# Performance work log

Measured on AMD Instinct MI355X. Metric: run time of the kernel, lower is better.

Reference implementation:

```python
import jax, jax.numpy as jnp
import numpy as np

EPS = 1e-12

def _normalize(x, axis=-1):
    # matches torch F.normalize(dim=-1) with default eps=1e-12
    n = jnp.linalg.norm(x, axis=axis, keepdims=True)
    return x / jnp.maximum(n, EPS)

def setup_inputs() -> dict:
    key = jax.random.key(0)
    k1, k2, k3 = jax.random.split(key, 3)
    B, D, C = 262144, 256, 128
    dirs = jax.random.normal(k1, (B, D), dtype=jnp.float32)
    v_class = _normalize(jax.random.normal(k2, (C, D), dtype=jnp.float32))
    labels = jax.random.randint(k3, (B,), 0, C, dtype=jnp.int32)
    return {"dirs": dirs, "v_class": v_class, "labels": labels, "step": 100}

def reference(dirs, v_class, labels, step):
    n_classes, _ = v_class.shape
    ema_alpha = 0.02
    proto_weight = 0.1

    dirs_n = _normalize(dirs)                      # (B, D)

    # ---- EMA update (no-grad in original; segment-mean per class) ----
    d = jax.lax.stop_gradient(dirs_n)
    sums = jax.ops.segment_sum(d, labels, num_segments=n_classes)      # (C, D)
    counts = jax.ops.segment_sum(jnp.ones((d.shape[0],), d.dtype), labels,
                                 num_segments=n_classes)               # (C,)
    batch_mean = sums / jnp.maximum(counts, 1.0)[:, None]
    batch_mean = _normalize(batch_mean)
    alpha = min(ema_alpha, step / (step + 50))
    updated = _normalize((1.0 - alpha) * v_class + alpha * batch_mean)
    new_v = jnp.where((counts > 0)[:, None], updated, v_class)         # (C, D)
    new_v = jax.lax.stop_gradient(new_v)  # buffer: no grad flows through it

    # ---- prototype alignment loss ----
    protos = new_v[labels]                          # (B, D) gather
    cos_sim = jnp.sum(dirs_n * protos, axis=-1)     # (B,)
    l_proto = jnp.mean(1.0 - cos_sim)
    return proto_weight * l_proto, new_v
```

## Files before the change

### kernel.cpp

```cpp
#include <hip/hip_runtime.h>


#define PF_D 256
#define PF_C 128
#define PF_SCALE 524288.0f
#define PF_INV_SCALE (1.0f / 524288.0f)

__device__ __forceinline__ float pf_wave_sum(float v) {
  #pragma unroll
  for (int m = 1; m < 64; m <<= 1) v += __shfl_xor(v, m, 64);
  return v;
}

__global__ void pf_zero(int* __restrict__ ws, int n) {
  int i = blockIdx.x * blockDim.x + threadIdx.x;
  if (i < n) ws[i] = 0;
}

__global__ __launch_bounds__(1024) void pf_accum(
    const float* __restrict__ dirs, const int* __restrict__ labels,
    int* __restrict__ gsum, int* __restrict__ gcnt, int B) {
  __shared__ int lacc[PF_C * PF_D];
  __shared__ int lnum[PF_C];
  const int tid = threadIdx.x;
  for (int i = tid; i < PF_C * PF_D; i += 1024) lacc[i] = 0;
  if (tid < PF_C) lnum[tid] = 0;
  __syncthreads();

  const int lane = tid & 63;
  const int wave = tid >> 6;
  const int rows_per_block = (B + (int)gridDim.x - 1) / (int)gridDim.x;
  const int row_lo = blockIdx.x * rows_per_block;
  const int row_hi = min(B, row_lo + rows_per_block);

  for (int r = row_lo + wave; r < row_hi; r += 16) {
    float4 v = ((const float4*)(dirs + (size_t)r * PF_D))[lane];
    float sq = v.x * v.x + v.y * v.y + v.z * v.z + v.w * v.w;
    sq = pf_wave_sum(sq);
    float k = PF_SCALE / fmaxf(sqrtf(sq), 1e-12f);
    int cls = labels[r];
    int* p = lacc + cls * PF_D;
    atomicAdd(p + lane,       __float2int_rn(v.x * k));
    atomicAdd(p + 64  + lane, __float2int_rn(v.y * k));
    atomicAdd(p + 128 + lane, __float2int_rn(v.z * k));
    atomicAdd(p + 192 + lane, __float2int_rn(v.w * k));
    if (lane == 0) atomicAdd(&lnum[cls], 1);
  }
  __syncthreads();

  for (int i = tid; i < PF_C * PF_D; i += 1024) {
    int s = lacc[i];
    if (s != 0) atomicAdd(&gsum[i], s);
  }
  if (tid < PF_C) {
    int s = lnum[tid];
    if (s != 0) atomicAdd(&gcnt[tid], s);
  }
}

__global__ __launch_bounds__(256) void pf_final(
    const int* __restrict__ gsum, const int* __restrict__ gcnt,
    const float* __restrict__ v_class, const int* __restrict__ step_ptr,
    float* __restrict__ out, int B) {
  const int lane = threadIdx.x & 63;
  const int wave = threadIdx.x >> 6;
  const float stepf = (float)step_ptr[0];
  const float alpha = fminf(0.02f, stepf / (stepf + 50.f));
  float acc = 0.f;

  for (int c = wave; c < PF_C; c += 4) {
    int   cnt   = gcnt[c];
    float denom = fmaxf((float)cnt, 1.f);
    float s[4], vc[4], bm[4];
    float nb = 0.f;
    #pragma unroll
    for (int j = 0; j < 4; j++) {
      int e = lane + 64 * j;
      s[j]  = (float)gsum[c * PF_D + ((e & 3) << 6) + (e >> 2)] * PF_INV_SCALE;
      vc[j] = v_class[c * PF_D + e];
      bm[j] = s[j] / denom;
      nb += bm[j] * bm[j];
    }
    nb = pf_wave_sum(nb);
    float rb = 1.f / fmaxf(sqrtf(nb), 1e-12f);
    float u[4];
    float nu = 0.f;
    #pragma unroll
    for (int j = 0; j < 4; j++) {
      u[j] = (1.f - alpha) * vc[j] + alpha * (bm[j] * rb);
      nu += u[j] * u[j];
    }
    nu = pf_wave_sum(nu);
    float ru = 1.f / fmaxf(sqrtf(nu), 1e-12f);
    #pragma unroll
    for (int j = 0; j < 4; j++) {
      int e = lane + 64 * j;
      float nv = (cnt > 0) ? u[j] * ru : vc[j];
      out[1 + c * PF_D + e] = nv;
      acc += s[j] * nv;
    }
  }

  acc = pf_wave_sum(acc);
  __shared__ float part[4];
  if (lane == 0) part[wave] = acc;
  __syncthreads();
  if (threadIdx.x == 0) {
    float tot = part[0] + part[1] + part[2] + part[3];
    out[0] = 0.1f * (1.f - tot / (float)B);
  }
}

extern "C" void kernel_launch(void* const* d_in, const int* in_sizes, int n_in,
                              void* d_out, int out_size, void* d_ws, size_t ws_size,
                              hipStream_t stream) {
  const float* dirs    = (const float*)d_in[0];
  const float* v_class = (const float*)d_in[1];
  const int*   labels  = (const int*)d_in[2];
  const int*   step    = (const int*)d_in[3];
  const int B = in_sizes[2];

  int* gsum = (int*)d_ws;
  int* gcnt = gsum + PF_C * PF_D;
  const int nzero = PF_C * PF_D + PF_C;

  pf_zero<<<(nzero + 255) / 256, 256, 0, stream>>>(gsum, nzero);
  pf_accum<<<256, 1024, 0, stream>>>(dirs, labels, gsum, gcnt, B);
  pf_final<<<1, 256, 0, stream>>>(gsum, gcnt, v_class, step,
                                  (float*)d_out, B);
}
```

Baseline: 427.3 us.

## Unroll accumulation over four rows per wave and split final stage across classes

The accumulation kernel now gives each wave a contiguous range of rows and handles four rows per iteration. The four loads, shuffle reductions and shared-memory atomics are interleaved to raise memory-level parallelism and hide latency. The single-block finalize is split into a per-class kernel with one wave per class, plus a tiny loss-reduction kernel, so the serial tail parallelizes across CUs. This adds an extra launch and more register pressure in the unrolled loop.

```diff
diff --git a/kernel.cpp b/kernel.cpp
--- a/kernel.cpp
+++ b/kernel.cpp
@@ -32,11 +32,61 @@
   const int rows_per_block = (B + (int)gridDim.x - 1) / (int)gridDim.x;
   const int row_lo = blockIdx.x * rows_per_block;
   const int row_hi = min(B, row_lo + rows_per_block);
+  const int rows_per_wave = (rows_per_block + 15) >> 4;
+  const int w_lo = row_lo + wave * rows_per_wave;
+  const int w_hi = min(row_hi, w_lo + rows_per_wave);
 
-  for (int r = row_lo + wave; r < row_hi; r += 16) {
+  int r = w_lo;
+  for (; r + 4 <= w_hi; r += 4) {
+    float4 v0 = ((const float4*)(dirs + (size_t)(r + 0) * PF_D))[lane];
+    float4 v1 = ((const float4*)(dirs + (size_t)(r + 1) * PF_D))[lane];
+    float4 v2 = ((const float4*)(dirs + (size_t)(r + 2) * PF_D))[lane];
+    float4 v3 = ((const float4*)(dirs + (size_t)(r + 3) * PF_D))[lane];
+    int c0 = labels[r + 0], c1 = labels[r + 1];
+    int c2 = labels[r + 2], c3 = labels[r + 3];
+    float s0 = v0.x * v0.x + v0.y * v0.y + v0.z * v0.z + v0.w * v0.w;
+    float s1 = v1.x * v1.x + v1.y * v1.y + v1.z * v1.z + v1.w * v1.w;
+    float s2 = v2.x * v2.x + v2.y * v2.y + v2.z * v2.z + v2.w * v2.w;
+    float s3 = v3.x * v3.x + v3.y * v3.y + v3.z * v3.z + v3.w * v3.w;
+    #pragma unroll
+    for (int m = 1; m < 64; m <<= 1) {
+      s0 += __shfl_xor(s0, m, 64);
+      s1 += __shfl_xor(s1, m, 64);
+      s2 += __shfl_xor(s2, m, 64);
+      s3 += __shfl_xor(s3, m, 64);
+    }
+    float k0 = PF_SCALE / fmaxf(sqrtf(s0), 1e-12f);
+    float k1 = PF_SCALE / fmaxf(sqrtf(s1), 1e-12f);
+    float k2 = PF_SCALE / fmaxf(sqrtf(s2), 1e-12f);
+    float k3 = PF_SCALE / fmaxf(sqrtf(s3), 1e-12f);
+    int* p0 = lacc + c0 * PF_D;
+    int* p1 = lacc + c1 * PF_D;
+    int* p2 = lacc + c2 * PF_D;
+    int* p3 = lacc + c3 * PF_D;
+    atomicAdd(p0 + lane,       __float2int_rn(v0.x * k0));
+    atomicAdd(p1 + lane,       __float2int_rn(v1.x * k1));
+    atomicAdd(p2 + lane,       __float2int_rn(v2.x * k2));
+    atomicAdd(p3 + lane,       __float2int_rn(v3.x * k3));
+    atomicAdd(p0 + 64 + lane,  __float2int_rn(v0.y * k0));
+    atomicAdd(p1 + 64 + lane,  __float2int_rn(v1.y * k1));
+    atomicAdd(p2 + 64 + lane,  __float2int_rn(v2.y * k2));
+    atomicAdd(p3 + 64 + lane,  __float2int_rn(v3.y * k3));
+    atomicAdd(p0 + 128 + lane, __float2int_rn(v0.z * k0));
+    atomicAdd(p1 + 128 + lane, __float2int_rn(v1.z * k1));
+    atomicAdd(p2 + 128 + lane, __float2int_rn(v2.z * k2));
+    atomicAdd(p3 + 128 + lane, __float2int_rn(v3.z * k3));
+    atomicAdd(p0 + 192 + lane, __float2int_rn(v0.w * k0));
+    atomicAdd(p1 + 192 + lane, __float2int_rn(v1.w * k1));
+    atomicAdd(p2 + 192 + lane, __float2int_rn(v2.w * k2));
+    atomicAdd(p3 + 192 + lane, __float2int_rn(v3.w * k3));
+    if (lane < 4) {
+      int cc = (lane == 0) ? c0 : (lane == 1) ? c1 : (lane == 2) ? c2 : c3;
+      atomicAdd(&lnum[cc], 1);
+    }
+  }
+  for (; r < w_hi; r++) {
     float4 v = ((const float4*)(dirs + (size_t)r * PF_D))[lane];
-    float sq = v.x * v.x + v.y * v.y + v.z * v.z + v.w * v.w;
-    sq = pf_wave_sum(sq);
+    float sq = pf_wave_sum(v.x * v.x + v.y * v.y + v.z * v.z + v.w * v.w);
     float k = PF_SCALE / fmaxf(sqrtf(sq), 1e-12f);
     int cls = labels[r];
     int* p = lacc + cls * PF_D;
@@ -58,57 +108,59 @@
   }
 }
 
-__global__ __launch_bounds__(256) void pf_final(
+__global__ __launch_bounds__(64) void pf_cls(
     const int* __restrict__ gsum, const int* __restrict__ gcnt,
     const float* __restrict__ v_class, const int* __restrict__ step_ptr,
-    float* __restrict__ out, int B) {
-  const int lane = threadIdx.x & 63;
-  const int wave = threadIdx.x >> 6;
+    float* __restrict__ out, float* __restrict__ dots) {
+  const int c = blockIdx.x;
+  const int lane = threadIdx.x;
   const float stepf = (float)step_ptr[0];
   const float alpha = fminf(0.02f, stepf / (stepf + 50.f));
-  float acc = 0.f;
 
-  for (int c = wave; c < PF_C; c += 4) {
-    int   cnt   = gcnt[c];
-    float denom = fmaxf((float)cnt, 1.f);
-    float s[4], vc[4], bm[4];
-    float nb = 0.f;
-    #pragma unroll
-    for (int j = 0; j < 4; j++) {
-      int e = lane + 64 * j;
-      s[j]  = (float)gsum[c * PF_D + ((e & 3) << 6) + (e >> 2)] * PF_INV_SCALE;
-      vc[j] = v_class[c * PF_D + e];
-      bm[j] = s[j] / denom;
-      nb += bm[j] * bm[j];
-    }
-    nb = pf_wave_sum(nb);
-    float rb = 1.f / fmaxf(sqrtf(nb), 1e-12f);
-    float u[4];
-    float nu = 0.f;
-    #pragma unroll
-    for (int j = 0; j < 4; j++) {
-      u[j] = (1.f - alpha) * vc[j] + alpha * (bm[j] * rb);
-      nu += u[j] * u[j];
-    }
-    nu = pf_wave_sum(nu);
-    float ru = 1.f / fmaxf(sqrtf(nu), 1e-12f);
-    #pragma unroll
-    for (int j = 0; j < 4; j++) {
-      int e = lane + 64 * j;
-      float nv = (cnt > 0) ? u[j] * ru : vc[j];
-      out[1 + c * PF_D + e] = nv;
-      acc += s[j] * nv;
-    }
+  const int cnt = gcnt[c];
+  const float denom = fmaxf((float)cnt, 1.f);
+  float s[4], vc[4], bm[4];
+  float nb = 0.f;
+  #pragma unroll
+  for (int j = 0; j < 4; j++) {
+    int e = lane + 64 * j;
+    s[j]  = (float)gsum[c * PF_D + ((e & 3) << 6) + (e >> 2)] * PF_INV_SCALE;
+    vc[j] = v_class[c * PF_D + e];
+    bm[j] = s[j] / denom;
+    nb += bm[j] * bm[j];
   }
+  nb = pf_wave_sum(nb);
+  const float rb = 1.f / fmaxf(sqrtf(nb), 1e-12f);
+  float u[4];
+  float nu = 0.f;
+  #pragma unroll
+  for (int j = 0; j < 4; j++) {
+    u[j] = (1.f - alpha) * vc[j] + alpha * (bm[j] * rb);
+    nu += u[j] * u[j];
+  }
+  nu = pf_wave_sum(nu);
+  const float ru = 1.f / fmaxf(sqrtf(nu), 1e-12f);
+  float dacc = 0.f;
+  #pragma unroll
+  for (int j = 0; j < 4; j++) {
+    int e = lane + 64 * j;
+    float nv = (cnt > 0) ? u[j] * ru : vc[j];
+    out[1 + c * PF_D + e] = nv;
+    dacc += s[j] * nv;
+  }
+  dacc = pf_wave_sum(dacc);
+  if (lane == 0) dots[c] = dacc;
+}
 
-  acc = pf_wave_sum(acc);
-  __shared__ float part[4];
-  if (lane == 0) part[wave] = acc;
+__global__ __launch_bounds__(128) void pf_loss(
+    const float* __restrict__ dots, float* __restrict__ out, int B) {
+  const int tid = threadIdx.x;
+  float v = dots[tid];
+  v = pf_wave_sum(v);
+  __shared__ float part[2];
+  if ((tid & 63) == 0) part[tid >> 6] = v;
   __syncthreads();
-  if (threadIdx.x == 0) {
-    float tot = part[0] + part[1] + part[2] + part[3];
-    out[0] = 0.1f * (1.f - tot / (float)B);
-  }
+  if (tid == 0) out[0] = 0.1f * (1.f - (part[0] + part[1]) / (float)B);
 }
 
 extern "C" void kernel_launch(void* const* d_in, const int* in_sizes, int n_in,
@@ -120,12 +172,14 @@
   const int*   step    = (const int*)d_in[3];
   const int B = in_sizes[2];
 
-  int* gsum = (int*)d_ws;
-  int* gcnt = gsum + PF_C * PF_D;
+  int*   gsum = (int*)d_ws;
+  int*   gcnt = gsum + PF_C * PF_D;
+  float* dots = (float*)(gcnt + PF_C);
   const int nzero = PF_C * PF_D + PF_C;
 
   pf_zero<<<(nzero + 255) / 256, 256, 0, stream>>>(gsum, nzero);
   pf_accum<<<256, 1024, 0, stream>>>(dirs, labels, gsum, gcnt, B);
-  pf_final<<<1, 256, 0, stream>>>(gsum, gcnt, v_class, step,
-                                  (float*)d_out, B);
+  pf_cls<<<PF_C, 64, 0, stream>>>(gsum, gcnt, v_class, step,
+                                  (float*)d_out, dots);
+  pf_loss<<<1, 128, 0, stream>>>(dots, (float*)d_out, B);
 }
```

Result: faster. 390.3 us (-8.7%).
